# Kernel optimization log

Hardware: AMD Instinct MI355X
Metric: run time of the kernel (lower is better)

## Reference

```python
import jax, jax.numpy as jnp
import numpy as np

V, E, DIN, DH = 8192, 4096, 512, 256
N_CLASSES = 2
EPS = 1e-5  # torch LayerNorm default
EDGE_P = 0.004  # ~33 nodes per hyperedge


def layernorm(x, g, b):
    m = jnp.mean(x, axis=-1, keepdims=True)
    v = jnp.mean((x - m) ** 2, axis=-1, keepdims=True)
    return (x - m) / jnp.sqrt(v + EPS) * g + b


def setup_inputs() -> dict:
    key = jax.random.key(0)
    ks = jax.random.split(key, 8)
    X = jax.random.normal(ks[0], (V, DIN), dtype=jnp.float32)
    # binary incidence matrix (|V|, |E|)
    H_inc = (jax.random.uniform(ks[1], (V, E)) < EDGE_P).astype(jnp.float32)
    Wp = jax.random.normal(ks[2], (DH, DIN), dtype=jnp.float32) * 0.02  # input_proj (no bias)
    W0 = jax.random.normal(ks[3], (DH, DH), dtype=jnp.float32) * 0.02
    W1 = jax.random.normal(ks[4], (DH, DH), dtype=jnp.float32) * 0.02
    g0 = jnp.ones((DH,), jnp.float32); b0 = jnp.zeros((DH,), jnp.float32)
    g1 = jnp.ones((DH,), jnp.float32); b1 = jnp.zeros((DH,), jnp.float32)
    Wc = jax.random.normal(ks[5], (N_CLASSES, DH), dtype=jnp.float32) * 0.02
    bc = jnp.zeros((N_CLASSES,), jnp.float32)
    return {"X": X, "H_inc": H_inc, "Wp": Wp, "W0": W0, "W1": W1,
            "g0": g0, "b0": b0, "g1": g1, "b1": b1, "Wc": Wc, "bc": bc}


def reference(X, H_inc, Wp, W0, W1, g0, b0, g1, b1, Wc, bc):
    # --- normalized incidence: H_tilde = D_v^{-1/2} H D_e^{-1/2}, 0 for isolated ---
    d_v = H_inc.sum(axis=1)   # (V,)
    d_e = H_inc.sum(axis=0)   # (E,)
    dvi = jnp.where(d_v > 0, jnp.where(d_v > 0, d_v, 1.0) ** -0.5, 0.0)
    dei = jnp.where(d_e > 0, jnp.where(d_e > 0, d_e, 1.0) ** -0.5, 0.0)
    H_tilde = dvi[:, None] * H_inc * dei[None, :]            # (V, E)
    HHt = H_tilde @ H_tilde.T                                # (V, V)

    # input projection
    Xh = X @ Wp.T                                            # (V, DH)

    # L=2 message-passing layers with residual + LayerNorm
    for W, g, b in ((W0, g0, b0), (W1, g1, b1)):
        Xn = jax.nn.relu((HHt @ Xh) @ W.T)
        Xh = layernorm(Xh + Xn, g, b)

    # mean pool per hyperedge (== Python loop over E in the original):
    # z_e = mean of member node embeddings; zeros for empty hyperedges
    cnt = jnp.where(d_e > 0, d_e, 1.0)[:, None]              # (E, 1)
    z_E = (H_inc.T @ Xh) / cnt                               # (E, DH)

    logits = z_E @ Wc.T + bc                                 # (E, 2)
    return jax.nn.softmax(logits, axis=1)
```

## Files before the change

kernel.cpp:

```cpp
#include <hip/hip_runtime.h>
#include <math.h>

#define NV 8192
#define NE 4096
#define DIN 512
#define DH 256
#define CAP_E 96
#define CAP_V 64

#define OFF_XH   0
#define OFF_Z    (OFF_XH + NV*DH)
#define OFF_Y    (OFF_Z  + NV*DH)
#define OFF_NCNT (OFF_Y  + NE*DH)
#define OFF_ECNT (OFF_NCNT + NV)
#define OFF_EL   (OFF_ECNT + NE*16)
#define OFF_NL   (OFF_EL + NE*CAP_E)
#define OFF_XHB  (OFF_NL + NV*CAP_V)

using bf16x8 = __attribute__((ext_vector_type(8))) short;
using f32x4  = __attribute__((ext_vector_type(4))) float;

__device__ inline unsigned short f2bf(float f) {
    union { float f; unsigned u; } v; v.f = f;
    unsigned r = v.u + 0x7FFF + ((v.u >> 16) & 1);
    return (unsigned short)(r >> 16);
}
__device__ inline float b2f(unsigned short s) {
    union { unsigned u; float f; } v; v.u = ((unsigned)s) << 16; return v.f;
}

union ScanProjSmem {
    struct { short As[2048]; short Bs[16384]; } g;
    struct { int lcnt; int lbuf[CAP_V]; } s;
};

__global__ __launch_bounds__(256) void scan_proj(const float* __restrict__ H,
                                                 const float* __restrict__ X,
                                                 const float* __restrict__ Wp,
                                                 float* __restrict__ Xh,
                                                 unsigned short* __restrict__ Xhb,
                                                 int* __restrict__ edge_cnt,
                                                 int* __restrict__ node_cnt,
                                                 int* __restrict__ edge_list,
                                                 int* __restrict__ node_list) {
    __shared__ ScanProjSmem sm;
    const int tid = threadIdx.x;
    if (blockIdx.x >= NV / 32) {
        int v = blockIdx.x - NV / 32;
        if (tid == 0) sm.s.lcnt = 0;
        __syncthreads();
        const float4* H4 = (const float4*)(H + (size_t)v * NE);
        float4 h0 = H4[tid * 4 + 0], h1 = H4[tid * 4 + 1];
        float4 h2 = H4[tid * 4 + 2], h3 = H4[tid * 4 + 3];
        float hv[16] = {h0.x, h0.y, h0.z, h0.w, h1.x, h1.y, h1.z, h1.w,
                        h2.x, h2.y, h2.z, h2.w, h3.x, h3.y, h3.z, h3.w};
        int myE[16]; int n = 0;
        int e0 = tid * 16;
#pragma unroll
        for (int j = 0; j < 16; ++j)
            if (hv[j] != 0.0f) myE[n++] = e0 + j;
        if (n > 0) {
            int s = atomicAdd(&sm.s.lcnt, n);
            for (int k = 0; k < n; ++k) {
                int ee = myE[k];
                if (s + k < CAP_V) sm.s.lbuf[s + k] = ee;
                int gc = atomicAdd(&edge_cnt[ee << 4], 1);
                if (gc < CAP_E) edge_list[ee * CAP_E + gc] = v;
            }
        }
        __syncthreads();
        int c = sm.s.lcnt;
        if (tid == 0) node_cnt[v] = c;
        int cc = min(c, CAP_V);
        for (int i = tid; i < cc; i += 256) node_list[v * CAP_V + i] = sm.s.lbuf[i];
        return;
    }
    const int K = DIN;
    const int lane = tid & 63;
    const int w    = tid >> 6;
    const int bm   = blockIdx.x * 32;
    const int swz  = lane ^ ((lane >> 3) & 6);
    float4 ar[2], br[16];
    {
        int i0 = tid, i1 = tid + 256;
        ar[0] = *(const float4*)(X + (size_t)(bm + (i0 >> 4)) * K + ((i0 & 15) << 2));
        ar[1] = *(const float4*)(X + (size_t)(bm + (i1 >> 4)) * K + ((i1 & 15) << 2));
#pragma unroll
        for (int it = 0; it < 16; ++it) {
            int i = tid + it * 256;
            br[it] = *(const float4*)(Wp + (size_t)(i >> 4) * K + ((i & 15) << 2));
        }
    }
    f32x4 acc[2][4];
#pragma unroll
    for (int mi = 0; mi < 2; ++mi)
#pragma unroll
        for (int ni = 0; ni < 4; ++ni) acc[mi][ni] = (f32x4){0.f, 0.f, 0.f, 0.f};
    for (int k0 = 0; k0 < K; k0 += 64) {
        __syncthreads();
#pragma unroll
        for (int s = 0; s < 2; ++s) {
            int i = tid + s * 256;
            int row = i >> 4, kk = (i & 15) << 2;
            int kc = kk >> 5, quad = (kk >> 3) & 3, j = kk & 7;
            int ln = (row & 15) + (quad << 4);
            int pp = ln ^ ((ln >> 3) & 6);
            float4 v = ar[s];
            ushort4 u = {f2bf(v.x), f2bf(v.y), f2bf(v.z), f2bf(v.w)};
            *(ushort4*)&sm.g.As[((row >> 4) * 2 + kc) * 512 + pp * 8 + j] = u;
        }
#pragma unroll
        for (int it = 0; it < 16; ++it) {
            int i = tid + it * 256;
            int row = i >> 4, kk = (i & 15) << 2;
            int kc = kk >> 5, quad = (kk >> 3) & 3, j = kk & 7;
            int ln = (row & 15) + (quad << 4);
            int pp = ln ^ ((ln >> 3) & 6);
            float4 v = br[it];
            ushort4 u = {f2bf(v.x), f2bf(v.y), f2bf(v.z), f2bf(v.w)};
            *(ushort4*)&sm.g.Bs[((row >> 4) * 2 + kc) * 512 + pp * 8 + j] = u;
        }
        __syncthreads();
        if (k0 + 64 < K) {
            int kn = k0 + 64;
            int i0 = tid, i1 = tid + 256;
            ar[0] = *(const float4*)(X + (size_t)(bm + (i0 >> 4)) * K + kn + ((i0 & 15) << 2));
            ar[1] = *(const float4*)(X + (size_t)(bm + (i1 >> 4)) * K + kn + ((i1 & 15) << 2));
#pragma unroll
            for (int it = 0; it < 16; ++it) {
                int i = tid + it * 256;
                br[it] = *(const float4*)(Wp + (size_t)(i >> 4) * K + kn + ((i & 15) << 2));
            }
        }
#pragma unroll
        for (int kc = 0; kc < 2; ++kc) {
            bf16x8 af[2], bfr[4];
            af[0] = *(const bf16x8*)&sm.g.As[(0 * 2 + kc) * 512 + swz * 8];
            af[1] = *(const bf16x8*)&sm.g.As[(1 * 2 + kc) * 512 + swz * 8];
#pragma unroll
            for (int ni = 0; ni < 4; ++ni)
                bfr[ni] = *(const bf16x8*)&sm.g.Bs[((w * 4 + ni) * 2 + kc) * 512 + swz * 8];
#pragma unroll
            for (int mi = 0; mi < 2; ++mi)
#pragma unroll
                for (int ni = 0; ni < 4; ++ni)
                    acc[mi][ni] = __builtin_amdgcn_mfma_f32_16x16x32_bf16(
                        af[mi], bfr[ni], acc[mi][ni], 0, 0, 0);
        }
    }
    const int quad = lane >> 4, cl = lane & 15;
#pragma unroll
    for (int mi = 0; mi < 2; ++mi)
#pragma unroll
        for (int ni = 0; ni < 4; ++ni)
#pragma unroll
            for (int r = 0; r < 4; ++r) {
                float v = acc[mi][ni][r];
                size_t idx = (size_t)(bm + mi * 16 + quad * 4 + r) * DH + w * 64 + ni * 16 + cl;
                Xh[idx] = v;
                Xhb[idx] = f2bf(v);
            }
}

__global__ __launch_bounds__(256) void gemm_relu_res_ln(const float* __restrict__ Z,
                                                        const float* __restrict__ W,
                                                        float* __restrict__ Xh,
                                                        unsigned short* __restrict__ Xhb,
                                                        const float* __restrict__ g,
                                                        const float* __restrict__ b) {
    const int K = DH;
    __shared__ short As[2048];
    __shared__ short Bs[16384];
    __shared__ float redS[32][4];
    __shared__ float redQ[32][4];
    const int tid  = threadIdx.x;
    const int lane = tid & 63;
    const int w    = tid >> 6;
    const int bm   = blockIdx.x * 32;
    const int swz  = lane ^ ((lane >> 3) & 6);

    float4 ar[2], br[16];
    {
        int i0 = tid, i1 = tid + 256;
        ar[0] = *(const float4*)(Z + (size_t)(bm + (i0 >> 4)) * K + ((i0 & 15) << 2));
        ar[1] = *(const float4*)(Z + (size_t)(bm + (i1 >> 4)) * K + ((i1 & 15) << 2));
#pragma unroll
        for (int it = 0; it < 16; ++it) {
            int i = tid + it * 256;
            br[it] = *(const float4*)(W + (size_t)(i >> 4) * K + ((i & 15) << 2));
        }
    }
    f32x4 acc[2][4];
#pragma unroll
    for (int mi = 0; mi < 2; ++mi)
#pragma unroll
        for (int ni = 0; ni < 4; ++ni) acc[mi][ni] = (f32x4){0.f, 0.f, 0.f, 0.f};

    for (int k0 = 0; k0 < K; k0 += 64) {
        __syncthreads();
#pragma unroll
        for (int s = 0; s < 2; ++s) {
            int i = tid + s * 256;
            int row = i >> 4, kk = (i & 15) << 2;
            int kc = kk >> 5, quad = (kk >> 3) & 3, j = kk & 7;
            int ln = (row & 15) + (quad << 4);
            int pp = ln ^ ((ln >> 3) & 6);
            float4 v = ar[s];
            ushort4 u = {f2bf(v.x), f2bf(v.y), f2bf(v.z), f2bf(v.w)};
            *(ushort4*)&As[((row >> 4) * 2 + kc) * 512 + pp * 8 + j] = u;
        }
#pragma unroll
        for (int it = 0; it < 16; ++it) {
            int i = tid + it * 256;
            int row = i >> 4, kk = (i & 15) << 2;
            int kc = kk >> 5, quad = (kk >> 3) & 3, j = kk & 7;
            int ln = (row & 15) + (quad << 4);
            int pp = ln ^ ((ln >> 3) & 6);
            float4 v = br[it];
            ushort4 u = {f2bf(v.x), f2bf(v.y), f2bf(v.z), f2bf(v.w)};
            *(ushort4*)&Bs[((row >> 4) * 2 + kc) * 512 + pp * 8 + j] = u;
        }
        __syncthreads();
        if (k0 + 64 < K) {
            int kn = k0 + 64;
            int i0 = tid, i1 = tid + 256;
            ar[0] = *(const float4*)(Z + (size_t)(bm + (i0 >> 4)) * K + kn + ((i0 & 15) << 2));
            ar[1] = *(const float4*)(Z + (size_t)(bm + (i1 >> 4)) * K + kn + ((i1 & 15) << 2));
#pragma unroll
            for (int it = 0; it < 16; ++it) {
                int i = tid + it * 256;
                br[it] = *(const float4*)(W + (size_t)(i >> 4) * K + kn + ((i & 15) << 2));
            }
        }
#pragma unroll
        for (int kc = 0; kc < 2; ++kc) {
            bf16x8 af[2], bfr[4];
            af[0] = *(const bf16x8*)&As[(0 * 2 + kc) * 512 + swz * 8];
            af[1] = *(const bf16x8*)&As[(1 * 2 + kc) * 512 + swz * 8];
#pragma unroll
            for (int ni = 0; ni < 4; ++ni)
                bfr[ni] = *(const bf16x8*)&Bs[((w * 4 + ni) * 2 + kc) * 512 + swz * 8];
#pragma unroll
            for (int mi = 0; mi < 2; ++mi)
#pragma unroll
                for (int ni = 0; ni < 4; ++ni)
                    acc[mi][ni] = __builtin_amdgcn_mfma_f32_16x16x32_bf16(
                        af[mi], bfr[ni], acc[mi][ni], 0, 0, 0);
        }
    }
    const int quad = lane >> 4, cl = lane & 15;
#pragma unroll
    for (int mi = 0; mi < 2; ++mi)
#pragma unroll
        for (int r = 0; r < 4; ++r) {
            int row = bm + mi * 16 + quad * 4 + r;
            float s = 0.f, q = 0.f;
#pragma unroll
            for (int ni = 0; ni < 4; ++ni) {
                int col = w * 64 + ni * 16 + cl;
                float v = fmaxf(acc[mi][ni][r], 0.f) + Xh[(size_t)row * DH + col];
                acc[mi][ni][r] = v;
                s += v; q = fmaf(v, v, q);
            }
#pragma unroll
            for (int o = 1; o < 16; o <<= 1) {
                s += __shfl_xor(s, o, 64);
                q += __shfl_xor(q, o, 64);
            }
            if (cl == 0) {
                redS[mi * 16 + quad * 4 + r][w] = s;
                redQ[mi * 16 + quad * 4 + r][w] = q;
            }
        }
    __syncthreads();
#pragma unroll
    for (int mi = 0; mi < 2; ++mi)
#pragma unroll
        for (int r = 0; r < 4; ++r) {
            int R = mi * 16 + quad * 4 + r;
            float s = redS[R][0] + redS[R][1] + redS[R][2] + redS[R][3];
            float q = redQ[R][0] + redQ[R][1] + redQ[R][2] + redQ[R][3];
            float m = s * (1.0f / DH);
            float var = q * (1.0f / DH) - m * m;
            float rstd = rsqrtf(var + 1e-5f);
            int row = bm + R;
#pragma unroll
            for (int ni = 0; ni < 4; ++ni) {
                int col = w * 64 + ni * 16 + cl;
                float v = (acc[mi][ni][r] - m) * rstd * g[col] + b[col];
                size_t idx = (size_t)row * DH + col;
                Xh[idx] = v;
                Xhb[idx] = f2bf(v);
            }
        }
}

__global__ __launch_bounds__(64) void edge_gather(const unsigned short* __restrict__ Xhb,
                                                  const int* __restrict__ edge_cnt,
                                                  const int* __restrict__ edge_list,
                                                  const int* __restrict__ node_cnt,
                                                  float* __restrict__ Y) {
    int e = blockIdx.x;
    int tid = threadIdx.x;
    __shared__ int   lv[CAP_E];
    __shared__ float lc[CAP_E];
    int tc = edge_cnt[e << 4];
    int cnt = min(tc, CAP_E);
    for (int j = tid; j < cnt; j += 64) {
        int v = edge_list[e * CAP_E + j];
        lv[j] = v * (DH / 4);
        lc[j] = rsqrtf((float)node_cnt[v]);
    }
    __syncthreads();
    const ushort4* X4 = (const ushort4*)Xhb;
    float4 a[8];
#pragma unroll
    for (int u = 0; u < 8; ++u) a[u] = (float4){0.f, 0.f, 0.f, 0.f};
    int i = 0;
    for (; i + 8 <= cnt; i += 8) {
#pragma unroll
        for (int u = 0; u < 8; ++u) {
            ushort4 h = X4[lv[i + u] + tid]; float c = lc[i + u];
            a[u].x = fmaf(c, b2f(h.x), a[u].x); a[u].y = fmaf(c, b2f(h.y), a[u].y);
            a[u].z = fmaf(c, b2f(h.z), a[u].z); a[u].w = fmaf(c, b2f(h.w), a[u].w);
        }
    }
    for (; i < cnt; ++i) {
        ushort4 h = X4[lv[i] + tid]; float c = lc[i];
        a[0].x = fmaf(c, b2f(h.x), a[0].x); a[0].y = fmaf(c, b2f(h.y), a[0].y);
        a[0].z = fmaf(c, b2f(h.z), a[0].z); a[0].w = fmaf(c, b2f(h.w), a[0].w);
    }
#pragma unroll
    for (int u = 4; u > 0; u >>= 1)
#pragma unroll
        for (int q = 0; q < u; ++q) {
            a[q].x += a[q + u].x; a[q].y += a[q + u].y;
            a[q].z += a[q + u].z; a[q].w += a[q + u].w;
        }
    float de = tc > 0 ? rsqrtf((float)tc) : 0.f;
    float4 o = {de * a[0].x, de * a[0].y, de * a[0].z, de * a[0].w};
    ((float4*)Y)[e * (DH / 4) + tid] = o;
}

__global__ __launch_bounds__(64) void node_gather(const float* __restrict__ Y,
                                                  const int* __restrict__ node_cnt,
                                                  const int* __restrict__ node_list,
                                                  const int* __restrict__ edge_cnt,
                                                  float* __restrict__ Z) {
    int v = blockIdx.x;
    int tid = threadIdx.x;
    __shared__ int   le[CAP_V];
    __shared__ float lc[CAP_V];
    int tc = node_cnt[v];
    int cnt = min(tc, CAP_V);
    if (tid < cnt) {
        int e = node_list[v * CAP_V + tid];
        le[tid] = e * (DH / 4);
        lc[tid] = rsqrtf((float)edge_cnt[e << 4]);
    }
    __syncthreads();
    const float4* Y4 = (const float4*)Y;
    float4 a[8];
#pragma unroll
    for (int u = 0; u < 8; ++u) a[u] = (float4){0.f, 0.f, 0.f, 0.f};
    int i = 0;
    for (; i + 8 <= cnt; i += 8) {
#pragma unroll
        for (int u = 0; u < 8; ++u) {
            float4 x = Y4[le[i + u] + tid]; float c = lc[i + u];
            a[u].x = fmaf(c, x.x, a[u].x); a[u].y = fmaf(c, x.y, a[u].y);
            a[u].z = fmaf(c, x.z, a[u].z); a[u].w = fmaf(c, x.w, a[u].w);
        }
    }
    for (; i < cnt; ++i) {
        float4 x = Y4[le[i] + tid]; float c = lc[i];
        a[0].x = fmaf(c, x.x, a[0].x); a[0].y = fmaf(c, x.y, a[0].y);
        a[0].z = fmaf(c, x.z, a[0].z); a[0].w = fmaf(c, x.w, a[0].w);
    }
#pragma unroll
    for (int u = 4; u > 0; u >>= 1)
#pragma unroll
        for (int q = 0; q < u; ++q) {
            a[q].x += a[q + u].x; a[q].y += a[q + u].y;
            a[q].z += a[q + u].z; a[q].w += a[q + u].w;
        }
    float dv = tc > 0 ? rsqrtf((float)tc) : 0.f;
    float4 o = {dv * a[0].x, dv * a[0].y, dv * a[0].z, dv * a[0].w};
    ((float4*)Z)[v * (DH / 4) + tid] = o;
}

__global__ __launch_bounds__(64) void pool_classify(const float* __restrict__ Xh,
                                                    const int* __restrict__ edge_cnt,
                                                    const int* __restrict__ edge_list,
                                                    const float* __restrict__ Wc,
                                                    const float* __restrict__ bc,
                                                    float* __restrict__ out) {
    int e = blockIdx.x;
    int tid = threadIdx.x;
    __shared__ int lv[CAP_E];
    int tc = edge_cnt[e << 4];
    int cnt = min(tc, CAP_E);
    for (int j = tid; j < cnt; j += 64) lv[j] = edge_list[e * CAP_E + j] * (DH / 4);
    __syncthreads();
    const float4* X4 = (const float4*)Xh;
    float4 a[8];
#pragma unroll
    for (int u = 0; u < 8; ++u) a[u] = (float4){0, 0, 0, 0};
    int i = 0;
    for (; i + 8 <= cnt; i += 8) {
#pragma unroll
        for (int u = 0; u < 8; ++u) {
            float4 x = X4[lv[i + u] + tid];
            a[u].x += x.x; a[u].y += x.y; a[u].z += x.z; a[u].w += x.w;
        }
    }
    for (; i < cnt; ++i) {
        float4 x = X4[lv[i] + tid];
        a[0].x += x.x; a[0].y += x.y; a[0].z += x.z; a[0].w += x.w;
    }
#pragma unroll
    for (int u = 4; u > 0; u >>= 1)
#pragma unroll
        for (int q = 0; q < u; ++q) {
            a[q].x += a[q + u].x; a[q].y += a[q + u].y;
            a[q].z += a[q + u].z; a[q].w += a[q + u].w;
        }
    float inv = tc > 0 ? 1.0f / (float)tc : 1.0f;
    float4 val = {a[0].x * inv, a[0].y * inv, a[0].z * inv, a[0].w * inv};
    const float4* W4 = (const float4*)Wc;
    float4 w0 = W4[tid], w1 = W4[64 + tid];
    float p0 = val.x * w0.x + val.y * w0.y + val.z * w0.z + val.w * w0.w;
    float p1 = val.x * w1.x + val.y * w1.y + val.z * w1.z + val.w * w1.w;
#pragma unroll
    for (int o = 32; o > 0; o >>= 1) {
        p0 += __shfl_down(p0, o, 64);
        p1 += __shfl_down(p1, o, 64);
    }
    if (tid == 0) {
        float l0 = p0 + bc[0], l1 = p1 + bc[1];
        float mx = fmaxf(l0, l1);
        float e0 = expf(l0 - mx), e1 = expf(l1 - mx);
        float s = 1.0f / (e0 + e1);
        out[e * 2 + 0] = e0 * s;
        out[e * 2 + 1] = e1 * s;
    }
}

extern "C" void kernel_launch(void* const* d_in, const int* in_sizes, int n_in,
                              void* d_out, int out_size, void* d_ws, size_t ws_size,
                              hipStream_t stream) {
    const float* X  = (const float*)d_in[0];
    const float* H  = (const float*)d_in[1];
    const float* Wp = (const float*)d_in[2];
    const float* W0 = (const float*)d_in[3];
    const float* W1 = (const float*)d_in[4];
    const float* g0 = (const float*)d_in[5];
    const float* b0 = (const float*)d_in[6];
    const float* g1 = (const float*)d_in[7];
    const float* b1 = (const float*)d_in[8];
    const float* Wc = (const float*)d_in[9];
    const float* bc = (const float*)d_in[10];
    float* out = (float*)d_out;

    float* ws = (float*)d_ws;
    float* Xh  = ws + OFF_XH;
    float* Z   = ws + OFF_Z;
    float* Y   = ws + OFF_Y;
    int* node_cnt  = (int*)(ws + OFF_NCNT);
    int* edge_cnt  = (int*)(ws + OFF_ECNT);
    int* edge_list = (int*)(ws + OFF_EL);
    int* node_list = (int*)(ws + OFF_NL);
    unsigned short* Xhb = (unsigned short*)(ws + OFF_XHB);

    hipMemsetAsync(edge_cnt, 0, (size_t)(NE * 16) * sizeof(int), stream);

    scan_proj<<<NV / 32 + NV, 256, 0, stream>>>(H, X, Wp, Xh, Xhb,
                                                edge_cnt, node_cnt, edge_list, node_list);

    const float* Ws[2] = {W0, W1};
    const float* gs[2] = {g0, g1};
    const float* bs[2] = {b0, b1};
    for (int l = 0; l < 2; ++l) {
        edge_gather<<<NE, 64, 0, stream>>>(Xhb, edge_cnt, edge_list, node_cnt, Y);
        node_gather<<<NV, 64, 0, stream>>>(Y, node_cnt, node_list, edge_cnt, Z);
        gemm_relu_res_ln<<<NV / 32, 256, 0, stream>>>(Z, Ws[l], Xh, Xhb, gs[l], bs[l]);
    }

    pool_classify<<<NE, 64, 0, stream>>>(Xh, edge_cnt, edge_list, Wc, bc, out);
}
```

Before: 335.5 us.

## Scan one incidence row per wavefront and halve projection K-tile

The incidence scan now gives each wavefront its own node row, so a block handles four nodes. This cuts the scan grid fourfold and removes the block-wide barriers. The projection GEMM's K step drops from 64 to 32, which halves the shared-memory tiles and the prefetch registers, likely to improve occupancy. The cost is twice as many K iterations with more barriers, plus per-element shared atomics in the scan instead of one batched atomic per thread.

Result: faster. 327.9 us (-2.3%).

```diff
diff --git a/kernel.cpp b/kernel.cpp
--- a/kernel.cpp
+++ b/kernel.cpp
@@ -7,6 +7,8 @@
 #define DH 256
 #define CAP_E 96
 #define CAP_V 64
+#define NPROJ (NV / 32)
+#define NSCAN (NV / 4)
 
 #define OFF_XH   0
 #define OFF_Z    (OFF_XH + NV*DH)
@@ -30,8 +32,8 @@
 }
 
 union ScanProjSmem {
-    struct { short As[2048]; short Bs[16384]; } g;
-    struct { int lcnt; int lbuf[CAP_V]; } s;
+    struct { short As[1024]; short Bs[8192]; } g;
+    struct { int lcnt[4]; int lbuf[4][CAP_V]; } s;
 };
 
 __global__ __launch_bounds__(256) void scan_proj(const float* __restrict__ H,
@@ -45,34 +47,32 @@
                                                  int* __restrict__ node_list) {
     __shared__ ScanProjSmem sm;
     const int tid = threadIdx.x;
-    if (blockIdx.x >= NV / 32) {
-        int v = blockIdx.x - NV / 32;
-        if (tid == 0) sm.s.lcnt = 0;
-        __syncthreads();
+    if (blockIdx.x >= NPROJ) {
+        const int w = tid >> 6, lane = tid & 63;
+        const int v = (blockIdx.x - NPROJ) * 4 + w;
+        if (lane == 0) sm.s.lcnt[w] = 0;
         const float4* H4 = (const float4*)(H + (size_t)v * NE);
-        float4 h0 = H4[tid * 4 + 0], h1 = H4[tid * 4 + 1];
-        float4 h2 = H4[tid * 4 + 2], h3 = H4[tid * 4 + 3];
-        float hv[16] = {h0.x, h0.y, h0.z, h0.w, h1.x, h1.y, h1.z, h1.w,
-                        h2.x, h2.y, h2.z, h2.w, h3.x, h3.y, h3.z, h3.w};
-        int myE[16]; int n = 0;
-        int e0 = tid * 16;
-#pragma unroll
-        for (int j = 0; j < 16; ++j)
-            if (hv[j] != 0.0f) myE[n++] = e0 + j;
-        if (n > 0) {
-            int s = atomicAdd(&sm.s.lcnt, n);
-            for (int k = 0; k < n; ++k) {
-                int ee = myE[k];
-                if (s + k < CAP_V) sm.s.lbuf[s + k] = ee;
-                int gc = atomicAdd(&edge_cnt[ee << 4], 1);
-                if (gc < CAP_E) edge_list[ee * CAP_E + gc] = v;
-            }
-        }
-        __syncthreads();
-        int c = sm.s.lcnt;
-        if (tid == 0) node_cnt[v] = c;
+        float4 h[16];
+#pragma unroll
+        for (int it = 0; it < 16; ++it) h[it] = H4[lane + 64 * it];
+#pragma unroll
+        for (int it = 0; it < 16; ++it) {
+            float hv[4] = {h[it].x, h[it].y, h[it].z, h[it].w};
+#pragma unroll
+            for (int c = 0; c < 4; ++c) {
+                if (hv[c] != 0.0f) {
+                    int ee = 256 * it + 4 * lane + c;
+                    int s = atomicAdd(&sm.s.lcnt[w], 1);
+                    if (s < CAP_V) sm.s.lbuf[w][s] = ee;
+                    int gc = atomicAdd(&edge_cnt[ee << 4], 1);
+                    if (gc < CAP_E) edge_list[ee * CAP_E + gc] = v;
+                }
+            }
+        }
+        int c = sm.s.lcnt[w];
+        if (lane == 0) node_cnt[v] = c;
         int cc = min(c, CAP_V);
-        for (int i = tid; i < cc; i += 256) node_list[v * CAP_V + i] = sm.s.lbuf[i];
+        for (int i = lane; i < cc; i += 64) node_list[v * CAP_V + i] = sm.s.lbuf[w][i];
         return;
     }
     const int K = DIN;
@@ -80,73 +80,61 @@
     const int w    = tid >> 6;
     const int bm   = blockIdx.x * 32;
     const int swz  = lane ^ ((lane >> 3) & 6);
-    float4 ar[2], br[16];
-    {
-        int i0 = tid, i1 = tid + 256;
-        ar[0] = *(const float4*)(X + (size_t)(bm + (i0 >> 4)) * K + ((i0 & 15) << 2));
-        ar[1] = *(const float4*)(X + (size_t)(bm + (i1 >> 4)) * K + ((i1 & 15) << 2));
-#pragma unroll
-        for (int it = 0; it < 16; ++it) {
-            int i = tid + it * 256;
-            br[it] = *(const float4*)(Wp + (size_t)(i >> 4) * K + ((i & 15) << 2));
-        }
+    float4 ar, br[8];
+    ar = *(const float4*)(X + (size_t)(bm + (tid >> 3)) * K + ((tid & 7) << 2));
+#pragma unroll
+    for (int it = 0; it < 8; ++it) {
+        int i = tid + it * 256;
+        br[it] = *(const float4*)(Wp + (size_t)(i >> 3) * K + ((i & 7) << 2));
     }
     f32x4 acc[2][4];
 #pragma unroll
     for (int mi = 0; mi < 2; ++mi)
 #pragma unroll
         for (int ni = 0; ni < 4; ++ni) acc[mi][ni] = (f32x4){0.f, 0.f, 0.f, 0.f};
-    for (int k0 = 0; k0 < K; k0 += 64) {
+    for (int k0 = 0; k0 < K; k0 += 32) {
         __syncthreads();
-#pragma unroll
-        for (int s = 0; s < 2; ++s) {
-            int i = tid + s * 256;
-            int row = i >> 4, kk = (i & 15) << 2;
-            int kc = kk >> 5, quad = (kk >> 3) & 3, j = kk & 7;
+        {
+            int row = tid >> 3, kk = (tid & 7) << 2;
+            int quad = kk >> 3, j = kk & 7;
             int ln = (row & 15) + (quad << 4);
             int pp = ln ^ ((ln >> 3) & 6);
-            float4 v = ar[s];
-            ushort4 u = {f2bf(v.x), f2bf(v.y), f2bf(v.z), f2bf(v.w)};
-            *(ushort4*)&sm.g.As[((row >> 4) * 2 + kc) * 512 + pp * 8 + j] = u;
-        }
-#pragma unroll
-        for (int it = 0; it < 16; ++it) {
+            ushort4 u = {f2bf(ar.x), f2bf(ar.y), f2bf(ar.z), f2bf(ar.w)};
+            *(ushort4*)&sm.g.As[(row >> 4) * 512 + pp * 8 + j] = u;
+        }
+#pragma unroll
+        for (int it = 0; it < 8; ++it) {
             int i = tid + it * 256;
-            int row = i >> 4, kk = (i & 15) << 2;
-            int kc = kk >> 5, quad = (kk >> 3) & 3, j = kk & 7;
+            int row = i >> 3, kk = (i & 7) << 2;
+            int quad = kk >> 3, j = kk & 7;
             int ln = (row & 15) + (quad << 4);
             int pp = ln ^ ((ln >> 3) & 6);
             float4 v = br[it];
             ushort4 u = {f2bf(v.x), f2bf(v.y), f2bf(v.z), f2bf(v.w)};
-            *(ushort4*)&sm.g.Bs[((row >> 4) * 2 + kc) * 512 + pp * 8 + j] = u;
+            *(ushort4*)&sm.g.Bs[(row >> 4) * 512 + pp * 8 + j] = u;
         }
         __syncthreads();
-        if (k0 + 64 < K) {
-            int kn = k0 + 64;
-            int i0 = tid, i1 = tid + 256;
-            ar[0] = *(const float4*)(X + (size_t)(bm + (i0 >> 4)) * K + kn + ((i0 & 15) << 2));
-            ar[1] = *(const float4*)(X + (size_t)(bm + (i1 >> 4)) * K + kn + ((i1 & 15) << 2));
-#pragma unroll
-            for (int it = 0; it < 16; ++it) {
+        if (k0 + 32 < K) {
+            int kn = k0 + 32;
+            ar = *(const float4*)(X + (size_t)(bm + (tid >> 3)) * K + kn + ((tid & 7) << 2));
+#pragma unroll
+            for (int it = 0; it < 8; ++it) {
                 int i = tid + it * 256;
-                br[it] = *(const float4*)(Wp + (size_t)(i >> 4) * K + kn + ((i & 15) << 2));
-            }
-        }
-#pragma unroll
-        for (int kc = 0; kc < 2; ++kc) {
-            bf16x8 af[2], bfr[4];
-            af[0] = *(const bf16x8*)&sm.g.As[(0 * 2 + kc) * 512 + swz * 8];
-            af[1] = *(const bf16x8*)&sm.g.As[(1 * 2 + kc) * 512 + swz * 8];
+                br[it] = *(const float4*)(Wp + (size_t)(i >> 3) * K + kn + ((i & 7) << 2));
+            }
+        }
+        bf16x8 af[2], bfr[4];
+        af[0] = *(const bf16x8*)&sm.g.As[0 * 512 + swz * 8];
+        af[1] = *(const bf16x8*)&sm.g.As[1 * 512 + swz * 8];
+#pragma unroll
+        for (int ni = 0; ni < 4; ++ni)
+            bfr[ni] = *(const bf16x8*)&sm.g.Bs[(w * 4 + ni) * 512 + swz * 8];
+#pragma unroll
+        for (int mi = 0; mi < 2; ++mi)
 #pragma unroll
             for (int ni = 0; ni < 4; ++ni)
-                bfr[ni] = *(const bf16x8*)&sm.g.Bs[((w * 4 + ni) * 2 + kc) * 512 + swz * 8];
-#pragma unroll
-            for (int mi = 0; mi < 2; ++mi)
-#pragma unroll
-                for (int ni = 0; ni < 4; ++ni)
-                    acc[mi][ni] = __builtin_amdgcn_mfma_f32_16x16x32_bf16(
-                        af[mi], bfr[ni], acc[mi][ni], 0, 0, 0);
-        }
+                acc[mi][ni] = __builtin_amdgcn_mfma_f32_16x16x32_bf16(
+                    af[mi], bfr[ni], acc[mi][ni], 0, 0, 0);
     }
     const int quad = lane >> 4, cl = lane & 15;
 #pragma unroll
@@ -474,8 +462,8 @@
 
     hipMemsetAsync(edge_cnt, 0, (size_t)(NE * 16) * sizeof(int), stream);
 
-    scan_proj<<<NV / 32 + NV, 256, 0, stream>>>(H, X, Wp, Xh, Xhb,
-                                                edge_cnt, node_cnt, edge_list, node_list);
+    scan_proj<<<NPROJ + NSCAN, 256, 0, stream>>>(H, X, Wp, Xh, Xhb,
+                                                 edge_cnt, node_cnt, edge_list, node_list);
 
     const float* Ws[2] = {W0, W1};
     const float* gs[2] = {g0, g1};
```
